# Performance work log

Measured on AMD Instinct MI355X. Metric: run time of the kernel, lower is better.

Reference implementation:

```python
import jax, jax.numpy as jnp
import numpy as np

# Regular (dv=3, dc=6) LDPC Tanner graph, rate 1/2
N = 2097152   # variable nodes (code.n)
M = 1048576   # check nodes (H.shape[0])
DV = 3
DC = 6
T = 10        # max_iterations
BC = 4        # c2v bit-width -> 2^(bc-1) = 8 magnitude levels
K = 2 ** (BC - 1)
QUANT_PARAMS = [(2.0, 1.0), (4.0, 1.5), (6.0, 2.0)]


def _make_thresholds():
    """Per-iteration threshold table [T, K]; tau_j = C*(j/(K-1))**gamma."""
    def thr(C, g):
        return [C * (j / (K - 1)) ** g for j in range(K)]
    rows = []
    for t in range(T):
        if t < T // 3:
            C, g = QUANT_PARAMS[0]
        elif t < 2 * T // 3:
            C, g = QUANT_PARAMS[1]
        else:
            C, g = QUANT_PARAMS[-1]
        rows.append(thr(C, g))
    return jnp.asarray(rows, dtype=jnp.float32)


def setup_inputs() -> dict:
    key = jax.random.key(0)
    k_llr, k_beta, k_alpha = jax.random.split(key, 3)
    rng = np.random.default_rng(0)
    # each variable node has exactly DV edges; each check exactly DC edges
    var_idx = np.repeat(np.arange(N, dtype=np.int32), DV)
    chk_idx = rng.permutation(np.repeat(np.arange(M, dtype=np.int32), DC)).astype(np.int32)
    llr = jax.random.normal(k_llr, (N,), dtype=jnp.float32) * 2.0
    # weight init matches nn.Parameter(torch.randn(1)*0.1), one per (iter, degree)
    beta = jax.random.normal(k_beta, (T,), dtype=jnp.float32) * 0.1
    alpha = jax.random.normal(k_alpha, (T,), dtype=jnp.float32) * 0.1
    return {
        "llr": llr,
        "var_idx": jnp.asarray(var_idx),
        "chk_idx": jnp.asarray(chk_idx),
        "beta": beta,
        "alpha": alpha,
        "thresholds": _make_thresholds(),
        "m": M,
    }


def reference(llr, var_idx, chk_idx, beta, alpha, thresholds, m):
    n = llr.shape[0]
    E = var_idx.shape[0]
    eidx = jnp.arange(E, dtype=jnp.int32)
    INF = jnp.float32(jnp.inf)

    def step(v2c, xs):
        b, a, thr = xs  # scalar beta_t, alpha_t, thr [K]
        neg = v2c < 0
        sgn = jnp.where(neg, -1.0, 1.0).astype(v2c.dtype)
        mag = jnp.abs(v2c)
        # --- check node update: min-sum with exclusion (min1/min2) ---
        min1 = jax.ops.segment_min(mag, chk_idx, num_segments=m)
        # first edge attaining the min in each check (ties -> lowest edge id)
        cand = jnp.where(mag <= min1[chk_idx], eidx, E)
        first = jax.ops.segment_min(cand, chk_idx, num_segments=m)
        is_min = eidx == first[chk_idx]
        min2 = jax.ops.segment_min(jnp.where(is_min, INF, mag), chk_idx, num_segments=m)
        min2 = jnp.where(jnp.isinf(min2), min1, min2)  # degree-1 guard
        # sign product excluding self: total parity * own sign
        cnt = jax.ops.segment_sum(neg.astype(jnp.int32), chk_idx, num_segments=m)
        tot = (1 - 2 * (cnt & 1)).astype(v2c.dtype)
        sign_excl = tot[chk_idx] * sgn
        mval = jnp.where(is_min, min2[chk_idx], min1[chk_idx])
        raw = b * sign_excl * mval
        # --- RCQ quantize/dequantize of c2v: snap |raw| down to threshold ---
        q = jnp.clip(jnp.searchsorted(thr, jnp.abs(raw), side="right") - 1, 0, K - 1)
        c2v = jnp.where(raw < 0, -1.0, 1.0) * thr[q]
        # --- variable node update ---
        post = llr + jax.ops.segment_sum(c2v, var_idx, num_segments=n)
        v2c_new = a * (post[var_idx] - c2v)
        return v2c_new, post

    v2c0 = llr[var_idx]
    _, posts = jax.lax.scan(step, v2c0, (beta, alpha, thresholds))
    posterior = posts[-1]
    decoded = (posterior < 0).astype(jnp.int32)
    return decoded, posterior, jnp.int32(beta.shape[0])
```

## Files before the change

### kernel.cpp

```cpp
#include <hip/hip_runtime.h>
#include <stdint.h>

#define NV 2097152
#define MC 1048576
#define EE 6291456
#define TT 10

#define CHUNK 8192
#define NBLK 768
#define FBK 512
#define CPB 2048
#define CSEG 12288
#define FG 512
#define GSEG 12288
#define VBK 256
#define VSEG 24576

__global__ __launch_bounds__(512) void initcur_kernel(uint32_t* __restrict__ gcur) {
    int i = blockIdx.x * 512 + threadIdx.x;
    gcur[i] = (uint32_t)(i & 511) * 12288u;
}

__global__ __launch_bounds__(256) void bin1_kernel(const int* __restrict__ chk_idx,
                                                   uint32_t* __restrict__ gcurA,
                                                   uint32_t* __restrict__ im1_e,
                                                   uint16_t* __restrict__ im1_c) {
    __shared__ uint32_t cnt[2][512];
    __shared__ uint32_t scanv[512];
    __shared__ uint32_t adj[512];
    __shared__ uint32_t sA[CHUNK];
    __shared__ uint16_t sB[CHUNK];
    const int tid = threadIdx.x;
    const int rep = tid >> 7;
    const int base = blockIdx.x * CHUNK;
    cnt[0][tid] = 0; cnt[0][tid + 256] = 0;
    cnt[1][tid] = 0; cnt[1][tid + 256] = 0;
    __syncthreads();
    int4 cc4[8];
#pragma unroll
    for (int k = 0; k < 8; ++k) cc4[k] = ((const int4*)chk_idx)[(base >> 2) + tid + 256 * k];
    uint32_t br[32];
#pragma unroll
    for (int k = 0; k < 8; ++k) {
        int cv[4] = {cc4[k].x, cc4[k].y, cc4[k].z, cc4[k].w};
#pragma unroll
        for (int ii = 0; ii < 4; ++ii) {
            uint32_t b = (uint32_t)cv[ii] >> 11;
            uint32_t r = atomicAdd(&cnt[rep][b], 1u);
            br[k * 4 + ii] = (b << 13) | r;
        }
    }
    __syncthreads();
    uint32_t s0 = cnt[0][tid] + cnt[1][tid];
    uint32_t s1 = cnt[0][tid + 256] + cnt[1][tid + 256];
    scanv[tid] = s0; scanv[tid + 256] = s1;
    __syncthreads();
    for (int d = 1; d < 512; d <<= 1) {
        uint32_t a0 = (tid >= d) ? scanv[tid - d] : 0u;
        uint32_t a1 = scanv[tid + 256 - d];
        __syncthreads();
        scanv[tid] += a0; scanv[tid + 256] += a1;
        __syncthreads();
    }
    scanv[tid] -= s0; scanv[tid + 256] -= s1;
    adj[tid] = atomicAdd(&gcurA[tid], s0) - scanv[tid];
    adj[tid + 256] = atomicAdd(&gcurA[tid + 256], s1) - scanv[tid + 256];
    __syncthreads();
#pragma unroll
    for (int k = 0; k < 8; ++k) {
        int cv[4] = {cc4[k].x, cc4[k].y, cc4[k].z, cc4[k].w};
#pragma unroll
        for (int ii = 0; ii < 4; ++ii) {
            uint32_t v = br[k * 4 + ii];
            uint32_t b = v >> 13;
            uint32_t r = v & 8191u;
            uint32_t j = scanv[b] + (rep ? cnt[0][b] : 0u) + r;
            uint32_t e = (uint32_t)(base + (tid + 256 * k) * 4 + ii);
            sA[j] = (b << 23) | e;
            sB[j] = (uint16_t)((uint32_t)cv[ii] & 2047u);
        }
    }
    __syncthreads();
    for (int k = 0; k < 32; ++k) {
        int j = tid + 256 * k;
        uint32_t v = sA[j];
        uint32_t b = v >> 23;
        uint32_t addr = adj[b] + (uint32_t)j;
        im1_e[addr] = v & 0x7FFFFFu;
        im1_c[addr] = sB[j];
    }
}

__global__ __launch_bounds__(256) void place1_kernel(const uint32_t* __restrict__ im1_e,
                                                     const uint16_t* __restrict__ im1_c,
                                                     uint32_t* __restrict__ chk_edges,
                                                     uint8_t* __restrict__ b1rank,
                                                     uint32_t* __restrict__ runcntB) {
    __shared__ uint32_t win[CSEG];
    __shared__ uint32_t ccnt[CPB];
    __shared__ uint32_t cntB[VBK];
    const int tid = threadIdx.x, blk = blockIdx.x;
    for (int j = tid; j < CPB; j += 256) ccnt[j] = 0;
    cntB[tid] = 0;
    __syncthreads();
    const size_t cb = (size_t)blk * CSEG;
    for (int k = 0; k < 12; ++k) {
        int j0 = (tid + 256 * k) * 4;
        const uint4 e4 = *(const uint4*)&im1_e[cb + j0];
        const ushort4 c4 = *(const ushort4*)&im1_c[cb + j0];
        uint32_t s;
        s = atomicAdd(&ccnt[c4.x], 1u); win[c4.x * 6 + s] = e4.x;
        s = atomicAdd(&ccnt[c4.y], 1u); win[c4.y * 6 + s] = e4.y;
        s = atomicAdd(&ccnt[c4.z], 1u); win[c4.z * 6 + s] = e4.z;
        s = atomicAdd(&ccnt[c4.w], 1u); win[c4.w * 6 + s] = e4.w;
    }
    __syncthreads();
    for (int j = tid; j < CSEG; j += 256) chk_edges[cb + j] = win[j];
    for (int k = 0; k < CSEG / 256; ++k) {
        int lp = tid + 256 * k;
        uint32_t e = win[lp];
        uint32_t bB = (e / 3u) >> 13;
        uint32_t r = atomicAdd(&cntB[bB], 1u);
        b1rank[cb + lp] = (uint8_t)r;
    }
    __syncthreads();
    runcntB[(size_t)tid * FBK + blk] = cntB[tid];
}

__global__ __launch_bounds__(256) void bin2_kernel(const uint32_t* __restrict__ chk_edges,
                                                   uint32_t* __restrict__ gcurB,
                                                   uint32_t* __restrict__ im2_pay,
                                                   uint16_t* __restrict__ im2_el) {
    __shared__ uint32_t cnt[2][512];
    __shared__ uint32_t scanv[512];
    __shared__ uint32_t adj[512];
    __shared__ uint32_t sA[CHUNK];
    __shared__ uint16_t sB[CHUNK];
    const int tid = threadIdx.x;
    const int rep = tid >> 7;
    const int base = blockIdx.x * CHUNK;
    cnt[0][tid] = 0; cnt[0][tid + 256] = 0;
    cnt[1][tid] = 0; cnt[1][tid + 256] = 0;
    __syncthreads();
    uint4 ee4[8];
#pragma unroll
    for (int k = 0; k < 8; ++k) ee4[k] = ((const uint4*)chk_edges)[(base >> 2) + tid + 256 * k];
    uint32_t br[32];
#pragma unroll
    for (int k = 0; k < 8; ++k) {
        uint32_t ev[4] = {ee4[k].x, ee4[k].y, ee4[k].z, ee4[k].w};
#pragma unroll
        for (int ii = 0; ii < 4; ++ii) {
            uint32_t vb = ev[ii] / 12288u;
            uint32_t r = atomicAdd(&cnt[rep][vb], 1u);
            br[k * 4 + ii] = (vb << 13) | r;
        }
    }
    __syncthreads();
    uint32_t s0 = cnt[0][tid] + cnt[1][tid];
    uint32_t s1 = cnt[0][tid + 256] + cnt[1][tid + 256];
    scanv[tid] = s0; scanv[tid + 256] = s1;
    __syncthreads();
    for (int d = 1; d < 512; d <<= 1) {
        uint32_t a0 = (tid >= d) ? scanv[tid - d] : 0u;
        uint32_t a1 = scanv[tid + 256 - d];
        __syncthreads();
        scanv[tid] += a0; scanv[tid + 256] += a1;
        __syncthreads();
    }
    scanv[tid] -= s0; scanv[tid + 256] -= s1;
    adj[tid] = atomicAdd(&gcurB[tid], s0) - scanv[tid];
    adj[tid + 256] = atomicAdd(&gcurB[tid + 256], s1) - scanv[tid + 256];
    __syncthreads();
#pragma unroll
    for (int k = 0; k < 8; ++k) {
        uint32_t ev[4] = {ee4[k].x, ee4[k].y, ee4[k].z, ee4[k].w};
#pragma unroll
        for (int ii = 0; ii < 4; ++ii) {
            uint32_t v = br[k * 4 + ii];
            uint32_t vb = v >> 13;
            uint32_t r = v & 8191u;
            uint32_t j = scanv[vb] + (rep ? cnt[0][vb] : 0u) + r;
            uint32_t pl = (uint32_t)((tid + 256 * k) * 4 + ii);
            sA[j] = (vb << 13) | pl;
            sB[j] = (uint16_t)(ev[ii] - vb * 12288u);
        }
    }
    __syncthreads();
    for (int k = 0; k < 32; ++k) {
        int j = tid + 256 * k;
        uint32_t v = sA[j];
        uint32_t vb = v >> 13;
        uint32_t pos = (uint32_t)base + (v & 8191u);
        uint32_t c = pos / 6u;
        uint32_t s = pos - c * 6u;
        uint32_t addr = adj[vb] + (uint32_t)j;
        im2_pay[addr] = (c << 3) | s;
        im2_el[addr] = sB[j];
    }
}

__global__ __launch_bounds__(256) void place2_kernel(const uint32_t* __restrict__ im2_pay,
                                                     const uint16_t* __restrict__ im2_el,
                                                     uint32_t* __restrict__ dest,
                                                     uint8_t* __restrict__ f1rank,
                                                     uint32_t* __restrict__ runcntF) {
    __shared__ uint32_t win2[GSEG];
    __shared__ uint32_t cntF[FBK];
    const int tid = threadIdx.x, g = blockIdx.x;
    cntF[tid] = 0; cntF[tid + 256] = 0;
    __syncthreads();
    const size_t gb = (size_t)g * GSEG;
    for (int k = 0; k < 12; ++k) {
        int j0 = (tid + 256 * k) * 4;
        const uint4 p4 = *(const uint4*)&im2_pay[gb + j0];
        const ushort4 e4 = *(const ushort4*)&im2_el[gb + j0];
        win2[e4.x] = p4.x; win2[e4.y] = p4.y; win2[e4.z] = p4.z; win2[e4.w] = p4.w;
    }
    __syncthreads();
    for (int j = tid; j < GSEG; j += 256) dest[gb + j] = win2[j];
    for (int k = 0; k < GSEG / 256; ++k) {
        int le = tid + 256 * k;
        uint32_t b = (win2[le] >> 3) >> 11;
        uint32_t r = atomicAdd(&cntF[b], 1u);
        f1rank[gb + le] = (uint8_t)r;
    }
    __syncthreads();
    runcntF[(size_t)tid * FG + g] = cntF[tid];
    runcntF[(size_t)(tid + 256) * FG + g] = cntF[tid + 256];
}

__global__ void scanF_kernel(const uint32_t* __restrict__ runcntF,
                             uint32_t* __restrict__ f1base) {
    int b = blockIdx.x * 256 + threadIdx.x;
    uint32_t acc = (uint32_t)b * CSEG;
    for (int g = 0; g < FG; ++g) {
        f1base[(size_t)g * FBK + b] = acc;
        acc += runcntF[(size_t)b * FG + g];
    }
}

__global__ void scanB_kernel(const uint32_t* __restrict__ runcntB,
                             uint32_t* __restrict__ b1base) {
    int bB = threadIdx.x;
    uint32_t acc = (uint32_t)bB * VSEG;
    for (int blk = 0; blk < FBK; ++blk) {
        b1base[(size_t)blk * VBK + bB] = acc;
        acc += runcntB[(size_t)bB * FBK + blk];
    }
}

__global__ __launch_bounds__(256) void fb_kernel(const uint32_t* __restrict__ dest,
                                                 const uint8_t* __restrict__ f1rank,
                                                 const uint32_t* __restrict__ runcntF,
                                                 const uint32_t* __restrict__ f1base,
                                                 uint32_t* __restrict__ goffF,
                                                 uint16_t* __restrict__ f2pos,
                                                 uint16_t* __restrict__ bidxF,
                                                 uint16_t* __restrict__ lvF) {
    __shared__ uint32_t flb[FBK];
    __shared__ uint32_t rowf[FBK];
    __shared__ uint32_t sortv[GSEG];
    const int tid = threadIdx.x, g = blockIdx.x;
    uint32_t c0 = runcntF[(size_t)tid * FG + g];
    uint32_t c1 = runcntF[(size_t)(tid + 256) * FG + g];
    flb[tid] = c0; flb[tid + 256] = c1;
    rowf[tid] = f1base[(size_t)g * FBK + tid];
    rowf[tid + 256] = f1base[(size_t)g * FBK + tid + 256];
    __syncthreads();
    for (int d = 1; d < FBK; d <<= 1) {
        uint32_t a0 = (tid >= d) ? flb[tid - d] : 0u;
        uint32_t a1 = flb[tid + 256 - d];
        __syncthreads();
        flb[tid] += a0; flb[tid + 256] += a1;
        __syncthreads();
    }
    flb[tid] -= c0; flb[tid + 256] -= c1;
    __syncthreads();
    goffF[(size_t)g * FBK + tid] = rowf[tid] - flb[tid];
    goffF[(size_t)g * FBK + tid + 256] = rowf[tid + 256] - flb[tid + 256];
    const size_t gb = (size_t)g * GSEG;
    for (int k = 0; k < GSEG / 256; ++k) {
        int le = tid + 256 * k;
        uint32_t d = dest[gb + le];
        uint32_t r = f1rank[gb + le];
        uint32_t c = d >> 3;
        uint32_t b = c >> 11;
        uint32_t pl = c * 6u + (d & 7u) - b * 12288u;
        sortv[flb[b] + r] = (b << 14) | pl;
    }
    __syncthreads();
    for (int k = 0; k < GSEG / 256; ++k) {
        int j = tid + 256 * k;
        uint32_t v = sortv[j];
        uint32_t b = v >> 14;
        f2pos[rowf[b] - flb[b] + j] = (uint16_t)(v & 16383u);
        bidxF[gb + j] = (uint16_t)b;
    }
    __syncthreads();
    for (int k = 0; k < GSEG / 256; ++k) {
        int le = tid + 256 * k;
        uint32_t d = dest[gb + le];
        uint32_t r = f1rank[gb + le];
        uint32_t b = (d >> 3) >> 11;
        sortv[flb[b] + r] = (uint32_t)(le / 3);
    }
    __syncthreads();
    for (int k = 0; k < GSEG / 256; ++k) {
        int j = tid + 256 * k;
        lvF[gb + j] = (uint16_t)sortv[j];
    }
}

__global__ __launch_bounds__(256) void bb_kernel(const uint32_t* __restrict__ chk_edges,
                                                 const uint8_t* __restrict__ b1rank,
                                                 const uint32_t* __restrict__ runcntB,
                                                 const uint32_t* __restrict__ b1base,
                                                 uint32_t* __restrict__ goffB,
                                                 uint16_t* __restrict__ b2pos,
                                                 uint8_t* __restrict__ bidxB,
                                                 uint16_t* __restrict__ lposB) {
    __shared__ uint32_t blb[VBK];
    __shared__ uint32_t rowb[VBK];
    __shared__ uint32_t sortv[CSEG];
    const int tid = threadIdx.x, blk = blockIdx.x;
    uint32_t c0 = runcntB[(size_t)tid * FBK + blk];
    blb[tid] = c0;
    rowb[tid] = b1base[(size_t)blk * VBK + tid];
    __syncthreads();
    for (int d = 1; d < VBK; d <<= 1) {
        uint32_t a0 = (tid >= d) ? blb[tid - d] : 0u;
        __syncthreads();
        blb[tid] += a0;
        __syncthreads();
    }
    blb[tid] -= c0;
    __syncthreads();
    goffB[(size_t)blk * VBK + tid] = rowb[tid] - blb[tid];
    const size_t cb = (size_t)blk * CSEG;
    for (int k = 0; k < CSEG / 256; ++k) {
        int lp = tid + 256 * k;
        uint32_t e = chk_edges[cb + lp];
        uint32_t r = b1rank[cb + lp];
        uint32_t bB = (e / 3u) >> 13;
        uint32_t elocal = e - bB * VSEG;
        sortv[blb[bB] + r] = (bB << 15) | elocal;
    }
    __syncthreads();
    for (int k = 0; k < CSEG / 256; ++k) {
        int j = tid + 256 * k;
        uint32_t v = sortv[j];
        uint32_t bB = v >> 15;
        b2pos[rowb[bB] - blb[bB] + j] = (uint16_t)(v & 32767u);
        bidxB[cb + j] = (uint8_t)bB;
    }
    __syncthreads();
    for (int k = 0; k < CSEG / 256; ++k) {
        int lp = tid + 256 * k;
        uint32_t e = chk_edges[cb + lp];
        uint32_t r = b1rank[cb + lp];
        uint32_t bB = (e / 3u) >> 13;
        sortv[blb[bB] + r] = (uint32_t)lp;
    }
    __syncthreads();
    for (int k = 0; k < CSEG / 256; ++k) {
        int j = tid + 256 * k;
        lposB[cb + j] = (uint16_t)sortv[j];
    }
}

__global__ __launch_bounds__(256) void check_kernel(const float* __restrict__ finterm,
                                                    const uint16_t* __restrict__ f2pos,
                                                    uint32_t* __restrict__ einfo,
                                                    const uint16_t* __restrict__ lposB,
                                                    const uint8_t* __restrict__ bidxB,
                                                    const uint32_t* __restrict__ goffB,
                                                    uint8_t* __restrict__ binterm,
                                                    const float* __restrict__ beta,
                                                    const float* __restrict__ alpha,
                                                    const float* __restrict__ thresholds,
                                                    int t) {
    __shared__ __align__(16) float fwin[CSEG];
    __shared__ uint32_t grow[VBK];
    __shared__ float tp[8];
    uint32_t* ewin = (uint32_t*)fwin;
    const int tid = threadIdx.x, blk = blockIdx.x;
    if (tid < 8) tp[tid] = thresholds[((t > 0) ? (t - 1) : 0) * 8 + tid];
    grow[tid] = goffB[(size_t)blk * VBK + tid];
    const size_t cb = (size_t)blk * CSEG;
    for (int k = 0; k < 12; ++k) {
        int j0 = (tid + 256 * k) * 4;
        const float4 f4 = *(const float4*)&finterm[cb + j0];
        const ushort4 p4 = *(const ushort4*)&f2pos[cb + j0];
        fwin[p4.x] = f4.x; fwin[p4.y] = f4.y; fwin[p4.z] = f4.z; fwin[p4.w] = f4.w;
    }
    __syncthreads();

    const float aPrev = (t > 0) ? alpha[t - 1] : 1.0f;
    const float b = beta[t];
    const float* thc = thresholds + t * 8;
    const float th1 = thc[1], th2 = thc[2], th3 = thc[3], th4 = thc[4];
    const float th5 = thc[5], th6 = thc[6], th7 = thc[7];
    const uint32_t signb = (b < 0.0f) ? 1u : 0u;

    uint32_t wreg[8];
    for (int i = 0; i < 8; ++i) {
        int lc = tid + 256 * i;
        uint32_t wprev = (t > 0) ? einfo[blk * CPB + lc] : 0u;
        float mags[6];
        uint32_t sgn[6];
        uint32_t parity = 0;
        uint64_t minkey = ~0ull;
#pragma unroll
        for (int j = 0; j < 6; ++j) {
            float p = fwin[lc * 6 + j];
            uint32_t nib = (wprev >> (4 * j)) & 15u;
            float mg0 = tp[nib & 7u];
            float c2v = (nib & 8u) ? -mg0 : mg0;
            float x = aPrev * (p - c2v);
            uint32_t s = (x < 0.0f) ? 1u : 0u;
            parity ^= s;
            sgn[j] = s;
            float mg = fabsf(x);
            mags[j] = mg;
            uint64_t key = (((uint64_t)__float_as_uint(mg)) << 3) | (uint32_t)j;
            minkey = (key < minkey) ? key : minkey;
        }
        float min1 = __uint_as_float((uint32_t)(minkey >> 3));
        uint32_t fs = (uint32_t)(minkey & 7u);
        float min2 = INFINITY;
#pragma unroll
        for (int j = 0; j < 6; ++j) {
            if ((uint32_t)j != fs) min2 = fminf(min2, mags[j]);
        }
        float m1 = fabsf(b * min1);
        float m2 = fabsf(b * min2);
        uint32_t q1 = (uint32_t)(m1 >= th1) + (uint32_t)(m1 >= th2) + (uint32_t)(m1 >= th3)
                    + (uint32_t)(m1 >= th4) + (uint32_t)(m1 >= th5) + (uint32_t)(m1 >= th6)
                    + (uint32_t)(m1 >= th7);
        uint32_t q2 = (uint32_t)(m2 >= th1) + (uint32_t)(m2 >= th2) + (uint32_t)(m2 >= th3)
                    + (uint32_t)(m2 >= th4) + (uint32_t)(m2 >= th5) + (uint32_t)(m2 >= th6)
                    + (uint32_t)(m2 >= th7);
        uint32_t w = 0;
#pragma unroll
        for (int j = 0; j < 6; ++j) {
            uint32_t neg = signb ^ parity ^ sgn[j];
            uint32_t q = ((uint32_t)j == fs) ? q2 : q1;
            w |= ((neg << 3) | q) << (4 * j);
        }
        wreg[i] = w;
    }
    __syncthreads();
    for (int i = 0; i < 8; ++i) {
        int lc = tid + 256 * i;
        ewin[lc] = wreg[i];
        einfo[blk * CPB + lc] = wreg[i];
    }
    __syncthreads();
    for (int k = 0; k < 12; ++k) {
        int j0 = (tid + 256 * k) * 4;
        const ushort4 lp4 = *(const ushort4*)&lposB[cb + j0];
        const uchar4 b4 = *(const uchar4*)&bidxB[cb + j0];
        uint32_t lp, word;
        lp = lp4.x; word = ewin[lp / 6u];
        binterm[grow[b4.x] + j0 + 0] = (uint8_t)((word >> ((lp - 6u * (lp / 6u)) * 4u)) & 15u);
        lp = lp4.y; word = ewin[lp / 6u];
        binterm[grow[b4.y] + j0 + 1] = (uint8_t)((word >> ((lp - 6u * (lp / 6u)) * 4u)) & 15u);
        lp = lp4.z; word = ewin[lp / 6u];
        binterm[grow[b4.z] + j0 + 2] = (uint8_t)((word >> ((lp - 6u * (lp / 6u)) * 4u)) & 15u);
        lp = lp4.w; word = ewin[lp / 6u];
        binterm[grow[b4.w] + j0 + 3] = (uint8_t)((word >> ((lp - 6u * (lp / 6u)) * 4u)) & 15u);
    }
}

__global__ __launch_bounds__(512) void var_kernel(const float* __restrict__ llr,
                                                  const uint8_t* __restrict__ binterm,
                                                  const uint16_t* __restrict__ b2pos,
                                                  const uint16_t* __restrict__ lvF,
                                                  const uint16_t* __restrict__ bidxF,
                                                  const uint32_t* __restrict__ goffF,
                                                  float* __restrict__ finterm,
                                                  const float* __restrict__ thresholds,
                                                  int t, int mode,
                                                  float* __restrict__ out) {
    __shared__ uint8_t nwin[VSEG];
    __shared__ float pwin[8192];
    __shared__ uint32_t growF[FBK];
    __shared__ float tl[8];
    const int tid = threadIdx.x, vblk = blockIdx.x;
    if (tid < 8) tl[tid] = thresholds[t * 8 + tid];
    if (mode != 1) {
        const size_t vb = (size_t)vblk * VSEG;
        for (int k = 0; k < 12; ++k) {
            int i0 = (tid + 512 * k) * 4;
            const uchar4 n4 = *(const uchar4*)&binterm[vb + i0];
            const ushort4 p4 = *(const ushort4*)&b2pos[vb + i0];
            nwin[p4.x] = n4.x; nwin[p4.y] = n4.y; nwin[p4.z] = n4.z; nwin[p4.w] = n4.w;
        }
    }
    __syncthreads();
    for (int i = 0; i < 16; ++i) {
        int lv = tid + 512 * i;
        int v = vblk * 8192 + lv;
        float post;
        if (mode == 1) {
            post = llr[v];
        } else {
            uint32_t n0 = nwin[3 * lv], n1 = nwin[3 * lv + 1], n2 = nwin[3 * lv + 2];
            float c0 = (n0 & 8u) ? -tl[n0 & 7u] : tl[n0 & 7u];
            float c1 = (n1 & 8u) ? -tl[n1 & 7u] : tl[n1 & 7u];
            float c2 = (n2 & 8u) ? -tl[n2 & 7u] : tl[n2 & 7u];
            post = llr[v] + ((c0 + c1) + c2);
        }
        pwin[lv] = post;
        if (mode == 2) {
            out[v] = (post < 0.0f) ? 1.0f : 0.0f;
            out[NV + v] = post;
            if (v == 0) out[2 * NV] = 10.0f;
        }
    }
    __syncthreads();
    if (mode != 2) {
        for (int h = 0; h < 2; ++h) {
            int g = 2 * vblk + h;
            growF[tid] = goffF[(size_t)g * FBK + tid];
            __syncthreads();
            const size_t gb = (size_t)g * GSEG;
            for (int k = 0; k < 6; ++k) {
                int j0 = (tid + 512 * k) * 4;
                const ushort4 lv4 = *(const ushort4*)&lvF[gb + j0];
                const ushort4 b4 = *(const ushort4*)&bidxF[gb + j0];
                finterm[growF[b4.x] + j0 + 0] = pwin[h * 4096 + lv4.x];
                finterm[growF[b4.y] + j0 + 1] = pwin[h * 4096 + lv4.y];
                finterm[growF[b4.z] + j0 + 2] = pwin[h * 4096 + lv4.z];
                finterm[growF[b4.w] + j0 + 3] = pwin[h * 4096 + lv4.w];
            }
            __syncthreads();
        }
    }
}

extern "C" void kernel_launch(void* const* d_in, const int* in_sizes, int n_in,
                              void* d_out, int out_size, void* d_ws, size_t ws_size,
                              hipStream_t stream) {
    const float* llr        = (const float*)d_in[0];
    const int*   var_idx    = (const int*)d_in[1];   (void)var_idx;
    const int*   chk_idx    = (const int*)d_in[2];
    const float* beta       = (const float*)d_in[3];
    const float* alpha      = (const float*)d_in[4];
    const float* thresholds = (const float*)d_in[5];
    float* out = (float*)d_out;

    char* wsb = (char*)d_ws;
    float*    finterm   = (float*)(wsb + 0);
    uint16_t* f2pos     = (uint16_t*)(wsb + 25165824);
    uint16_t* lvF       = (uint16_t*)(wsb + 37748736);
    uint16_t* bidxF     = (uint16_t*)(wsb + 50331648);
    uint16_t* lposB     = (uint16_t*)(wsb + 62914560);
    uint16_t* b2pos     = (uint16_t*)(wsb + 75497472);
    uint8_t*  bidxB     = (uint8_t*)(wsb + 88080384);
    uint8_t*  binterm   = (uint8_t*)(wsb + 94371840);
    uint32_t* einfo     = (uint32_t*)(wsb + 100663296);
    uint32_t* chk_edges = (uint32_t*)(wsb + 104857600);
    uint32_t* dest      = (uint32_t*)(wsb + 130023424);
    uint32_t* im1_e     = (uint32_t*)(wsb + 155189248);
    uint16_t* im1_c     = (uint16_t*)(wsb + 180355072);
    uint32_t* im2_pay   = im1_e;
    uint16_t* im2_el    = im1_c;
    uint8_t*  f1rank    = (uint8_t*)(wsb + 192937984);
    uint8_t*  b1rank    = (uint8_t*)(wsb + 199229440);
    uint32_t* runcntF   = (uint32_t*)(wsb + 205520896);
    uint32_t* f1base    = (uint32_t*)(wsb + 206569472);
    uint32_t* runcntB   = (uint32_t*)(wsb + 207618048);
    uint32_t* b1base    = (uint32_t*)(wsb + 208142336);
    uint32_t* goffF     = (uint32_t*)(wsb + 208666624);
    uint32_t* goffB     = (uint32_t*)(wsb + 209715200);
    uint32_t* gcur      = (uint32_t*)(wsb + 210239488);
    uint32_t* gcurA     = gcur;
    uint32_t* gcurB     = gcur + 512;

    const int B = 256;
    initcur_kernel<<<2, 512, 0, stream>>>(gcur);
    bin1_kernel<<<NBLK, B, 0, stream>>>(chk_idx, gcurA, im1_e, im1_c);
    place1_kernel<<<FBK, B, 0, stream>>>(im1_e, im1_c, chk_edges, b1rank, runcntB);
    bin2_kernel<<<NBLK, B, 0, stream>>>(chk_edges, gcurB, im2_pay, im2_el);
    place2_kernel<<<FG, B, 0, stream>>>(im2_pay, im2_el, dest, f1rank, runcntF);
    scanF_kernel<<<2, B, 0, stream>>>(runcntF, f1base);
    fb_kernel<<<FG, B, 0, stream>>>(dest, f1rank, runcntF, f1base, goffF, f2pos, bidxF, lvF);
    scanB_kernel<<<1, B, 0, stream>>>(runcntB, b1base);
    bb_kernel<<<FBK, B, 0, stream>>>(chk_edges, b1rank, runcntB, b1base, goffB, b2pos, bidxB, lposB);
    var_kernel<<<VBK, 512, 0, stream>>>(llr, binterm, b2pos, lvF, bidxF, goffF,
                                        finterm, thresholds, 0, 1, out);

    for (int t = 0; t < TT; ++t) {
        check_kernel<<<FBK, B, 0, stream>>>(finterm, f2pos, einfo, lposB, bidxB, goffB,
                                            binterm, beta, alpha, thresholds, t);
        var_kernel<<<VBK, 512, 0, stream>>>(llr, binterm, b2pos, lvF, bidxF, goffF,
                                            finterm, thresholds, t,
                                            (t == TT - 1) ? 2 : 0, out);
    }
}
```

Baseline: 769.4 us.

## Cut shared memory in preprocessing and var kernels, parallelize prefix scans

The bin kernels drop their 16-bit shared staging arrays and re-read the check index or edge payload from global memory in the scatter loop, which lowers LDS use per block. place1 packs two 16-bit counters into each 32-bit shared atomic, halving the counter array. The serial scanF/scanB kernels, which ran on one or two blocks, become one-block-per-bin parallel Hillis-Steele scans. var_kernel processes its two halves in turn with a half-size posterior window, halving its shared footprint to raise occupancy, at the cost of extra syncs and extra global gathers.

```diff
diff --git a/kernel.cpp b/kernel.cpp
--- a/kernel.cpp
+++ b/kernel.cpp
@@ -29,7 +29,6 @@
     __shared__ uint32_t scanv[512];
     __shared__ uint32_t adj[512];
     __shared__ uint32_t sA[CHUNK];
-    __shared__ uint16_t sB[CHUNK];
     const int tid = threadIdx.x;
     const int rep = tid >> 7;
     const int base = blockIdx.x * CHUNK;
@@ -68,7 +67,6 @@
     __syncthreads();
 #pragma unroll
     for (int k = 0; k < 8; ++k) {
-        int cv[4] = {cc4[k].x, cc4[k].y, cc4[k].z, cc4[k].w};
 #pragma unroll
         for (int ii = 0; ii < 4; ++ii) {
             uint32_t v = br[k * 4 + ii];
@@ -77,17 +75,18 @@
             uint32_t j = scanv[b] + (rep ? cnt[0][b] : 0u) + r;
             uint32_t e = (uint32_t)(base + (tid + 256 * k) * 4 + ii);
             sA[j] = (b << 23) | e;
-            sB[j] = (uint16_t)((uint32_t)cv[ii] & 2047u);
-        }
-    }
-    __syncthreads();
+        }
+    }
+    __syncthreads();
+#pragma unroll 8
     for (int k = 0; k < 32; ++k) {
         int j = tid + 256 * k;
         uint32_t v = sA[j];
         uint32_t b = v >> 23;
+        uint32_t e = v & 0x7FFFFFu;
         uint32_t addr = adj[b] + (uint32_t)j;
-        im1_e[addr] = v & 0x7FFFFFu;
-        im1_c[addr] = sB[j];
+        im1_e[addr] = e;
+        im1_c[addr] = (uint16_t)((uint32_t)chk_idx[e] & 2047u);
     }
 }
 
@@ -97,10 +96,10 @@
                                                      uint8_t* __restrict__ b1rank,
                                                      uint32_t* __restrict__ runcntB) {
     __shared__ uint32_t win[CSEG];
-    __shared__ uint32_t ccnt[CPB];
+    __shared__ uint32_t ccnt[CPB / 2];
     __shared__ uint32_t cntB[VBK];
     const int tid = threadIdx.x, blk = blockIdx.x;
-    for (int j = tid; j < CPB; j += 256) ccnt[j] = 0;
+    for (int j = tid; j < CPB / 2; j += 256) ccnt[j] = 0;
     cntB[tid] = 0;
     __syncthreads();
     const size_t cb = (size_t)blk * CSEG;
@@ -108,11 +107,15 @@
         int j0 = (tid + 256 * k) * 4;
         const uint4 e4 = *(const uint4*)&im1_e[cb + j0];
         const ushort4 c4 = *(const ushort4*)&im1_c[cb + j0];
-        uint32_t s;
-        s = atomicAdd(&ccnt[c4.x], 1u); win[c4.x * 6 + s] = e4.x;
-        s = atomicAdd(&ccnt[c4.y], 1u); win[c4.y * 6 + s] = e4.y;
-        s = atomicAdd(&ccnt[c4.z], 1u); win[c4.z * 6 + s] = e4.z;
-        s = atomicAdd(&ccnt[c4.w], 1u); win[c4.w * 6 + s] = e4.w;
+        uint32_t c, old, s;
+        c = c4.x; old = atomicAdd(&ccnt[c >> 1], 1u << ((c & 1) * 16));
+        s = (old >> ((c & 1) * 16)) & 0xFFFFu; win[c * 6 + s] = e4.x;
+        c = c4.y; old = atomicAdd(&ccnt[c >> 1], 1u << ((c & 1) * 16));
+        s = (old >> ((c & 1) * 16)) & 0xFFFFu; win[c * 6 + s] = e4.y;
+        c = c4.z; old = atomicAdd(&ccnt[c >> 1], 1u << ((c & 1) * 16));
+        s = (old >> ((c & 1) * 16)) & 0xFFFFu; win[c * 6 + s] = e4.z;
+        c = c4.w; old = atomicAdd(&ccnt[c >> 1], 1u << ((c & 1) * 16));
+        s = (old >> ((c & 1) * 16)) & 0xFFFFu; win[c * 6 + s] = e4.w;
     }
     __syncthreads();
     for (int j = tid; j < CSEG; j += 256) chk_edges[cb + j] = win[j];
@@ -135,7 +138,6 @@
     __shared__ uint32_t scanv[512];
     __shared__ uint32_t adj[512];
     __shared__ uint32_t sA[CHUNK];
-    __shared__ uint16_t sB[CHUNK];
     const int tid = threadIdx.x;
     const int rep = tid >> 7;
     const int base = blockIdx.x * CHUNK;
@@ -174,7 +176,6 @@
     __syncthreads();
 #pragma unroll
     for (int k = 0; k < 8; ++k) {
-        uint32_t ev[4] = {ee4[k].x, ee4[k].y, ee4[k].z, ee4[k].w};
 #pragma unroll
         for (int ii = 0; ii < 4; ++ii) {
             uint32_t v = br[k * 4 + ii];
@@ -183,20 +184,22 @@
             uint32_t j = scanv[vb] + (rep ? cnt[0][vb] : 0u) + r;
             uint32_t pl = (uint32_t)((tid + 256 * k) * 4 + ii);
             sA[j] = (vb << 13) | pl;
-            sB[j] = (uint16_t)(ev[ii] - vb * 12288u);
-        }
-    }
-    __syncthreads();
+        }
+    }
+    __syncthreads();
+#pragma unroll 8
     for (int k = 0; k < 32; ++k) {
         int j = tid + 256 * k;
         uint32_t v = sA[j];
         uint32_t vb = v >> 13;
-        uint32_t pos = (uint32_t)base + (v & 8191u);
+        uint32_t pl = v & 8191u;
+        uint32_t pos = (uint32_t)base + pl;
         uint32_t c = pos / 6u;
         uint32_t s = pos - c * 6u;
+        uint32_t ev = chk_edges[pos];
         uint32_t addr = adj[vb] + (uint32_t)j;
         im2_pay[addr] = (c << 3) | s;
-        im2_el[addr] = sB[j];
+        im2_el[addr] = (uint16_t)(ev - vb * 12288u);
     }
 }
 
@@ -230,24 +233,44 @@
     runcntF[(size_t)(tid + 256) * FG + g] = cntF[tid + 256];
 }
 
-__global__ void scanF_kernel(const uint32_t* __restrict__ runcntF,
-                             uint32_t* __restrict__ f1base) {
-    int b = blockIdx.x * 256 + threadIdx.x;
-    uint32_t acc = (uint32_t)b * CSEG;
-    for (int g = 0; g < FG; ++g) {
-        f1base[(size_t)g * FBK + b] = acc;
-        acc += runcntF[(size_t)b * FG + g];
-    }
-}
-
-__global__ void scanB_kernel(const uint32_t* __restrict__ runcntB,
-                             uint32_t* __restrict__ b1base) {
-    int bB = threadIdx.x;
-    uint32_t acc = (uint32_t)bB * VSEG;
-    for (int blk = 0; blk < FBK; ++blk) {
-        b1base[(size_t)blk * VBK + bB] = acc;
-        acc += runcntB[(size_t)bB * FBK + blk];
-    }
+__global__ __launch_bounds__(256) void scanF_kernel(const uint32_t* __restrict__ runcntF,
+                                                    uint32_t* __restrict__ f1base) {
+    __shared__ uint32_t sc[512];
+    const int tid = threadIdx.x, b = blockIdx.x;
+    uint32_t c0 = runcntF[(size_t)b * FG + tid];
+    uint32_t c1 = runcntF[(size_t)b * FG + tid + 256];
+    sc[tid] = c0; sc[tid + 256] = c1;
+    __syncthreads();
+    for (int d = 1; d < 512; d <<= 1) {
+        uint32_t a0 = (tid >= d) ? sc[tid - d] : 0u;
+        uint32_t a1 = sc[tid + 256 - d];
+        __syncthreads();
+        sc[tid] += a0; sc[tid + 256] += a1;
+        __syncthreads();
+    }
+    uint32_t base = (uint32_t)b * CSEG;
+    f1base[(size_t)tid * FBK + b] = base + sc[tid] - c0;
+    f1base[(size_t)(tid + 256) * FBK + b] = base + sc[tid + 256] - c1;
+}
+
+__global__ __launch_bounds__(256) void scanB_kernel(const uint32_t* __restrict__ runcntB,
+                                                    uint32_t* __restrict__ b1base) {
+    __shared__ uint32_t sc[512];
+    const int tid = threadIdx.x, bB = blockIdx.x;
+    uint32_t c0 = runcntB[(size_t)bB * FBK + tid];
+    uint32_t c1 = runcntB[(size_t)bB * FBK + tid + 256];
+    sc[tid] = c0; sc[tid + 256] = c1;
+    __syncthreads();
+    for (int d = 1; d < 512; d <<= 1) {
+        uint32_t a0 = (tid >= d) ? sc[tid - d] : 0u;
+        uint32_t a1 = sc[tid + 256 - d];
+        __syncthreads();
+        sc[tid] += a0; sc[tid + 256] += a1;
+        __syncthreads();
+    }
+    uint32_t base = (uint32_t)bB * VSEG;
+    b1base[(size_t)tid * VBK + bB] = base + sc[tid] - c0;
+    b1base[(size_t)(tid + 256) * VBK + bB] = base + sc[tid + 256] - c1;
 }
 
 __global__ __launch_bounds__(256) void fb_kernel(const uint32_t* __restrict__ dest,
@@ -484,7 +507,7 @@
                                                   int t, int mode,
                                                   float* __restrict__ out) {
     __shared__ uint8_t nwin[VSEG];
-    __shared__ float pwin[8192];
+    __shared__ float pwin[4096];
     __shared__ uint32_t growF[FBK];
     __shared__ float tl[8];
     const int tid = threadIdx.x, vblk = blockIdx.x;
@@ -499,43 +522,42 @@
         }
     }
     __syncthreads();
-    for (int i = 0; i < 16; ++i) {
-        int lv = tid + 512 * i;
-        int v = vblk * 8192 + lv;
-        float post;
-        if (mode == 1) {
-            post = llr[v];
-        } else {
-            uint32_t n0 = nwin[3 * lv], n1 = nwin[3 * lv + 1], n2 = nwin[3 * lv + 2];
-            float c0 = (n0 & 8u) ? -tl[n0 & 7u] : tl[n0 & 7u];
-            float c1 = (n1 & 8u) ? -tl[n1 & 7u] : tl[n1 & 7u];
-            float c2 = (n2 & 8u) ? -tl[n2 & 7u] : tl[n2 & 7u];
-            post = llr[v] + ((c0 + c1) + c2);
-        }
-        pwin[lv] = post;
-        if (mode == 2) {
-            out[v] = (post < 0.0f) ? 1.0f : 0.0f;
-            out[NV + v] = post;
-            if (v == 0) out[2 * NV] = 10.0f;
-        }
-    }
-    __syncthreads();
-    if (mode != 2) {
-        for (int h = 0; h < 2; ++h) {
-            int g = 2 * vblk + h;
-            growF[tid] = goffF[(size_t)g * FBK + tid];
-            __syncthreads();
-            const size_t gb = (size_t)g * GSEG;
-            for (int k = 0; k < 6; ++k) {
-                int j0 = (tid + 512 * k) * 4;
-                const ushort4 lv4 = *(const ushort4*)&lvF[gb + j0];
-                const ushort4 b4 = *(const ushort4*)&bidxF[gb + j0];
-                finterm[growF[b4.x] + j0 + 0] = pwin[h * 4096 + lv4.x];
-                finterm[growF[b4.y] + j0 + 1] = pwin[h * 4096 + lv4.y];
-                finterm[growF[b4.z] + j0 + 2] = pwin[h * 4096 + lv4.z];
-                finterm[growF[b4.w] + j0 + 3] = pwin[h * 4096 + lv4.w];
+    for (int h = 0; h < 2; ++h) {
+        if (h == 1) __syncthreads();
+        for (int i = 0; i < 8; ++i) {
+            int lv = tid + 512 * i;
+            int lvfull = h * 4096 + lv;
+            int v = vblk * 8192 + lvfull;
+            float post;
+            if (mode == 1) {
+                post = llr[v];
+            } else {
+                uint32_t n0 = nwin[3 * lvfull], n1 = nwin[3 * lvfull + 1], n2 = nwin[3 * lvfull + 2];
+                float c0 = (n0 & 8u) ? -tl[n0 & 7u] : tl[n0 & 7u];
+                float c1 = (n1 & 8u) ? -tl[n1 & 7u] : tl[n1 & 7u];
+                float c2 = (n2 & 8u) ? -tl[n2 & 7u] : tl[n2 & 7u];
+                post = llr[v] + ((c0 + c1) + c2);
             }
-            __syncthreads();
+            pwin[lv] = post;
+            if (mode == 2) {
+                out[v] = (post < 0.0f) ? 1.0f : 0.0f;
+                out[NV + v] = post;
+                if (v == 0) out[2 * NV] = 10.0f;
+            }
+        }
+        if (mode == 2) continue;
+        const int g = 2 * vblk + h;
+        growF[tid] = goffF[(size_t)g * FBK + tid];
+        __syncthreads();
+        const size_t gb = (size_t)g * GSEG;
+        for (int k = 0; k < 6; ++k) {
+            int j0 = (tid + 512 * k) * 4;
+            const ushort4 lv4 = *(const ushort4*)&lvF[gb + j0];
+            const ushort4 b4 = *(const ushort4*)&bidxF[gb + j0];
+            finterm[growF[b4.x] + j0 + 0] = pwin[lv4.x];
+            finterm[growF[b4.y] + j0 + 1] = pwin[lv4.y];
+            finterm[growF[b4.z] + j0 + 2] = pwin[lv4.z];
+            finterm[growF[b4.w] + j0 + 3] = pwin[lv4.w];
         }
     }
 }
@@ -585,9 +607,9 @@
     place1_kernel<<<FBK, B, 0, stream>>>(im1_e, im1_c, chk_edges, b1rank, runcntB);
     bin2_kernel<<<NBLK, B, 0, stream>>>(chk_edges, gcurB, im2_pay, im2_el);
     place2_kernel<<<FG, B, 0, stream>>>(im2_pay, im2_el, dest, f1rank, runcntF);
-    scanF_kernel<<<2, B, 0, stream>>>(runcntF, f1base);
+    scanF_kernel<<<FBK, B, 0, stream>>>(runcntF, f1base);
     fb_kernel<<<FG, B, 0, stream>>>(dest, f1rank, runcntF, f1base, goffF, f2pos, bidxF, lvF);
-    scanB_kernel<<<1, B, 0, stream>>>(runcntB, b1base);
+    scanB_kernel<<<VBK, B, 0, stream>>>(runcntB, b1base);
     bb_kernel<<<FBK, B, 0, stream>>>(chk_edges, b1rank, runcntB, b1base, goffB, b2pos, bidxB, lposB);
     var_kernel<<<VBK, 512, 0, stream>>>(llr, binterm, b2pos, lvF, bidxF, goffF,
                                         finterm, thresholds, 0, 1, out);
```

After: 764.6 us. Within noise of the previous version (-0.6%).
